# Performance work log

Measured on AMD Instinct MI355X. Metric: run time of the kernel, lower is better.

Reference implementation:

```python
import jax, jax.numpy as jnp
import numpy as np

B, N, C = 8, 1024, 10
RADIUS = 0.04
CONSUME_RADIUS = 0.04
ACCEL_SCALE = 0.02
MAX_VEL = 0.02
MAX_POS = 1.0
EDGES_TO_STAY_ALIVE = 3
CONSUME_EDGES_REQ = 1
EPS = 1e-9


def setup_inputs() -> dict:
    key = jax.random.key(0)
    ks = jax.random.split(key, 6)
    pos = jax.random.uniform(ks[0], (B, N, 2), dtype=jnp.float32) * 2.0 - 1.0  # in [-1, 1]
    vel = jax.random.normal(ks[1], (B, N, 2), dtype=jnp.float32) * 0.01
    # channel 4: node type, 1 = living cell, 0 = food (as in graph.x[:,4]==0 for food)
    cell = (jax.random.uniform(ks[2], (B, N, 1)) < 0.8).astype(jnp.float32)
    rest = jax.random.normal(ks[3], (B, N, C - 5), dtype=jnp.float32) * 0.1
    x = jnp.concatenate([pos, vel, cell, rest], axis=-1)  # [B,N,10]
    W1 = jax.random.normal(ks[4], (14, 16), dtype=jnp.float32) * 0.3
    W2 = jax.random.normal(ks[5], (16, 7), dtype=jnp.float32) * 0.3
    b1 = jnp.zeros((16,), jnp.float32)
    b2 = jnp.zeros((7,), jnp.float32)
    return {"x": x, "W1": W1, "b1": b1, "W2": W2, "b2": b2}


def reference(x, W1, b1, W2, b2):
    pos = x[..., :2]          # [B,N,2]
    vel = x[..., 2:4]         # [B,N,2]
    is_cell = x[..., 4] > 0.5  # [B,N] bool; food nodes have type 0
    cf = is_cell.astype(x.dtype)[..., None]  # [B,N,1]

    # ---- add_edges: dynamic radius graph (dense per-graph form) ----
    rel = pos[:, None, :, :] - pos[:, :, None, :]   # rel[b,i,j] = pos_j - pos_i, [B,N,N,2]
    dist = jnp.sqrt(jnp.sum(rel * rel, axis=-1) + EPS)  # [B,N,N]
    adj = (dist < RADIUS) & (dist > 1e-6)           # no self-edges
    adjf = adj.astype(x.dtype)

    # edge_attr = [dist, dx, dy, type_of_target]  (edge_attr[:,3]==0 -> food edge)
    tgt_type = jnp.broadcast_to(x[:, None, :, 4], dist.shape)
    e = jnp.stack([dist, rel[..., 0], rel[..., 1], tgt_type], axis=-1)  # [B,N,N,4]

    # ---- message_pass: MLP(concat(edge_attr, x_j)) -> hidden -> 7, sum-aggregate ----
    W1e, W1x = W1[:4], W1[4:]  # split so x_j term is computed once per node
    h = jax.nn.relu(
        jnp.einsum('bije,eh->bijh', e, W1e)
        + jnp.einsum('bjc,ch->bjh', x, W1x)[:, None, :, :]
        + b1
    )  # [B,N,N,16]
    agg_h = jnp.einsum('bij,bijh->bih', adjf, h)  # masked aggregation [B,N,16]
    deg = adjf.sum(-1)                            # [B,N]
    out = jnp.einsum('bih,ho->bio', agg_h, W2) + deg[..., None] * b2  # [B,N,7]

    # ---- update_graph: masked velocity / position scatter update ----
    out = out * cf  # h = message_pass(graph) * c_mask
    acc = out[..., :2] * ACCEL_SCALE
    new_vel = jnp.clip(vel + acc, -MAX_VEL, MAX_VEL)
    new_vel = jnp.where(is_cell[..., None], new_vel, vel)
    new_pos = jnp.clip(pos + new_vel * cf, -MAX_POS, MAX_POS)
    new_pos = jnp.where(is_cell[..., None], new_pos, pos)

    # ---- remove_nodes: island cells + consumed food -> keep mask (fixed shape) ----
    dead = is_cell & (deg < EDGES_TO_STAY_ALIVE)
    near = ((dist < CONSUME_RADIUS) & (dist > 1e-6)).astype(x.dtype)
    cell_neighbors = jnp.einsum('bij,bj->bi', near, cf[..., 0])  # cells near each node
    consumed = (~is_cell) & (cell_neighbors >= CONSUME_EDGES_REQ)
    keep = ~(dead | consumed)

    new_x = jnp.concatenate([new_pos, new_vel, x[..., 4:]], axis=-1)
    new_x = new_x * keep.astype(x.dtype)[..., None]  # prune by zeroing (fixed shape)
    return new_x
```

## Files before the change

### kernel.cpp

```cpp
#include <hip/hip_runtime.h>
#include <math.h>

namespace {

constexpr int BB = 8;
constexpr int NN = 1024;
constexpr int CC = 10;
constexpr float RADIUS = 0.04f;
constexpr float ACCEL_SCALE = 0.02f;
constexpr float MAX_VEL = 0.02f;
constexpr float MAX_POS = 1.0f;
constexpr float EPS = 1e-9f;
constexpr float D2_PREFILTER = 0.0017f;

__global__ __launch_bounds__(512) void gnca_one(
    const float* __restrict__ x,
    const float* __restrict__ W1,
    const float* __restrict__ b1,
    const float* __restrict__ W2,
    const float* __restrict__ b2,
    float* __restrict__ out)
{
    __shared__ alignas(16) float2 raw2[NN * 5];
    __shared__ alignas(16) float2 pos2[NN];

    const int tid = threadIdx.x;
    const int blk = blockIdx.x;
    const int b = blk >> 5;
    const int row0 = (blk & 31) * 32;
    const int w   = tid >> 6;
    const int sub = tid & 63;
    const int hh  = sub & 15;

    const float b1h = b1[hh];
    const float w1d = W1[hh];
    const float w1x = W1[16 + hh];
    const float w1y = W1[32 + hh];
    const float w1t = W1[48 + hh];
    float w1c[CC];
#pragma unroll
    for (int c = 0; c < CC; ++c) w1c[c] = W1[(4 + c) * 16 + hh];
    const float w20 = W2[hh * 7 + 0];
    const float w21 = W2[hh * 7 + 1];

    const float* __restrict__ xb = x + (size_t)b * NN * CC;

    {
        const float4* __restrict__ src = (const float4*)xb;
        float4* __restrict__ dst = (float4*)raw2;
#pragma unroll
        for (int k = 0; k < 5; ++k) dst[k * 512 + tid] = src[k * 512 + tid];
    }
    __syncthreads();

    {
        const float4* __restrict__ r4 = (const float4*)raw2;
        const float4 r0 = r4[tid * 5 + 0];
        const float4 r2 = r4[tid * 5 + 2];
        ((float4*)pos2)[tid] = make_float4(r0.x, r0.y, r2.z, r2.w);
    }
    __syncthreads();

    const int ibase = row0 + w * 4;
    float2 pi[4];
#pragma unroll
    for (int r = 0; r < 4; ++r) pi[r] = pos2[ibase + r];

    float o0p[4] = {0.f, 0.f, 0.f, 0.f};
    float o1p[4] = {0.f, 0.f, 0.f, 0.f};
    float dgp[4] = {0.f, 0.f, 0.f, 0.f};
    float cnp[4] = {0.f, 0.f, 0.f, 0.f};

    for (int jj = 0; jj < 16; ++jj) {
        const float2 pj = pos2[(jj << 6) + sub];

#pragma unroll
        for (int r = 0; r < 4; ++r) {
            const float dx = pj.x - pi[r].x;
            const float dy = pj.y - pi[r].y;
            unsigned long long m = __ballot(dx * dx + dy * dy < D2_PREFILTER);

            while (m) {
                const int src = __builtin_ctzll(m);
                m &= (m - 1);
                const int bj = (jj << 6) + src;
                const float2 q0 = raw2[bj * 5 + 0];
                const float2 q1 = raw2[bj * 5 + 1];
                const float2 q2 = raw2[bj * 5 + 2];
                const float2 q3 = raw2[bj * 5 + 3];
                const float2 q4 = raw2[bj * 5 + 4];
                const float bx = q0.x - pi[r].x;
                const float by = q0.y - pi[r].y;
                const float d2 =
                    __fadd_rn(__fadd_rn(__fmul_rn(bx, bx), __fmul_rn(by, by)), EPS);
                const float dist = __fsqrt_rn(d2);
                if (dist < RADIUS) {
                    const float tgt = q2.x;
                    float v = b1h;
                    v = fmaf(q0.x, w1c[0], v);  v = fmaf(q0.y, w1c[1], v);
                    v = fmaf(q1.x, w1c[2], v);  v = fmaf(q1.y, w1c[3], v);
                    v = fmaf(q2.x, w1c[4], v);  v = fmaf(q2.y, w1c[5], v);
                    v = fmaf(q3.x, w1c[6], v);  v = fmaf(q3.y, w1c[7], v);
                    v = fmaf(q4.x, w1c[8], v);  v = fmaf(q4.y, w1c[9], v);
                    v = fmaf(tgt,  w1t, v);
                    v = fmaf(by,   w1y, v);
                    v = fmaf(bx,   w1x, v);
                    v = fmaf(dist, w1d, v);
                    v = fmaxf(v, 0.0f);
                    o0p[r] = fmaf(v, w20, o0p[r]);
                    o1p[r] = fmaf(v, w21, o1p[r]);
                    dgp[r] += 1.0f;
                    cnp[r] += (tgt > 0.5f) ? 1.0f : 0.0f;
                }
            }
        }
    }

#pragma unroll
    for (int mm = 1; mm < 16; mm <<= 1) {
#pragma unroll
        for (int r = 0; r < 4; ++r) {
            o0p[r] += __shfl_xor(o0p[r], mm, 64);
            o1p[r] += __shfl_xor(o1p[r], mm, 64);
        }
    }

    if (sub < 4) {
        float o0s = o0p[0], o1s = o1p[0], degs = dgp[0], cns = cnp[0];
        float2 pis = pi[0];
#pragma unroll
        for (int r = 1; r < 4; ++r) {
            if (sub == r) {
                o0s = o0p[r]; o1s = o1p[r]; degs = dgp[r]; cns = cnp[r];
                pis = pi[r];
            }
        }
        const int iu = ibase + sub;

        const float2 q1 = raw2[iu * 5 + 1];
        const float2 q2 = raw2[iu * 5 + 2];
        const float2 q3 = raw2[iu * 5 + 3];
        const float2 q4 = raw2[iu * 5 + 4];

        const float typ_i = q2.x;
        const bool is_cell = typ_i > 0.5f;

        float o0 = degs * b2[0] + o0s;
        float o1 = degs * b2[1] + o1s;
        if (!is_cell) { o0 = 0.0f; o1 = 0.0f; }

        float nvx = q1.x, nvy = q1.y;
        float npx = pis.x, npy = pis.y;
        if (is_cell) {
            nvx = fminf(fmaxf(q1.x + o0 * ACCEL_SCALE, -MAX_VEL), MAX_VEL);
            nvy = fminf(fmaxf(q1.y + o1 * ACCEL_SCALE, -MAX_VEL), MAX_VEL);
            npx = fminf(fmaxf(pis.x + nvx, -MAX_POS), MAX_POS);
            npy = fminf(fmaxf(pis.y + nvy, -MAX_POS), MAX_POS);
        }

        const bool dead     = is_cell && (degs < 3.0f);
        const bool consumed = (!is_cell) && (cns >= 1.0f);
        const float keep = (dead || consumed) ? 0.0f : 1.0f;

        float2* __restrict__ op2 = (float2*)(out + ((size_t)b * NN + iu) * CC);
        op2[0] = make_float2(npx * keep, npy * keep);
        op2[1] = make_float2(nvx * keep, nvy * keep);
        op2[2] = make_float2(typ_i * keep, q2.y * keep);
        op2[3] = make_float2(q3.x * keep, q3.y * keep);
        op2[4] = make_float2(q4.x * keep, q4.y * keep);
    }
}

}

extern "C" void kernel_launch(void* const* d_in, const int* in_sizes, int n_in,
                              void* d_out, int out_size, void* d_ws, size_t ws_size,
                              hipStream_t stream) {
    const float* x  = (const float*)d_in[0];
    const float* W1 = (const float*)d_in[1];
    const float* b1 = (const float*)d_in[2];
    const float* W2 = (const float*)d_in[3];
    const float* b2 = (const float*)d_in[4];
    float* out = (float*)d_out;

    gnca_one<<<dim3(256), dim3(512), 0, stream>>>(x, W1, b1, W2, b2, out);
}
```

Baseline: 13.39 us.

## Assign one row per wavefront and launch four times more blocks

Each wavefront now handles a single target row instead of four, and the grid grows from 256 to 1024 blocks, each covering 8 rows. Position loads for the column sweep are batched eight at a time so their latency overlaps the ballot work. This spreads the work over more of the GPU's compute units and shortens the serial per-wave loop. The cost is that each block still stages the whole 40KB graph into shared memory, so global-to-LDS traffic is four times higher, and the larger LDS footprint per row may limit occupancy.

```diff
diff --git a/kernel.cpp b/kernel.cpp
--- a/kernel.cpp
+++ b/kernel.cpp
@@ -26,8 +26,8 @@
 
     const int tid = threadIdx.x;
     const int blk = blockIdx.x;
-    const int b = blk >> 5;
-    const int row0 = (blk & 31) * 32;
+    const int b = blk >> 7;
+    const int row0 = (blk & 127) * 8;
     const int w   = tid >> 6;
     const int sub = tid & 63;
     const int hh  = sub & 15;
@@ -61,23 +61,24 @@
     }
     __syncthreads();
 
-    const int ibase = row0 + w * 4;
-    float2 pi[4];
-#pragma unroll
-    for (int r = 0; r < 4; ++r) pi[r] = pos2[ibase + r];
+    const int iu = row0 + w;
+    const float2 pi = pos2[iu];
 
-    float o0p[4] = {0.f, 0.f, 0.f, 0.f};
-    float o1p[4] = {0.f, 0.f, 0.f, 0.f};
-    float dgp[4] = {0.f, 0.f, 0.f, 0.f};
-    float cnp[4] = {0.f, 0.f, 0.f, 0.f};
-
-    for (int jj = 0; jj < 16; ++jj) {
-        const float2 pj = pos2[(jj << 6) + sub];
+    float o0p = 0.0f, o1p = 0.0f, dg = 0.0f, cn = 0.0f;
 
 #pragma unroll
-        for (int r = 0; r < 4; ++r) {
-            const float dx = pj.x - pi[r].x;
-            const float dy = pj.y - pi[r].y;
+    for (int g = 0; g < 2; ++g) {
+        float2 pjv[8];
+#pragma unroll
+        for (int q = 0; q < 8; ++q)
+            pjv[q] = pos2[(((g << 3) + q) << 6) + sub];
+
+#pragma unroll
+        for (int q = 0; q < 8; ++q) {
+            const int jj = (g << 3) + q;
+            const float2 pj = pjv[q];
+            const float dx = pj.x - pi.x;
+            const float dy = pj.y - pi.y;
             unsigned long long m = __ballot(dx * dx + dy * dy < D2_PREFILTER);
 
             while (m) {
@@ -89,8 +90,8 @@
                 const float2 q2 = raw2[bj * 5 + 2];
                 const float2 q3 = raw2[bj * 5 + 3];
                 const float2 q4 = raw2[bj * 5 + 4];
-                const float bx = q0.x - pi[r].x;
-                const float by = q0.y - pi[r].y;
+                const float bx = q0.x - pi.x;
+                const float by = q0.y - pi.y;
                 const float d2 =
                     __fadd_rn(__fadd_rn(__fmul_rn(bx, bx), __fmul_rn(by, by)), EPS);
                 const float dist = __fsqrt_rn(d2);
@@ -107,10 +108,10 @@
                     v = fmaf(bx,   w1x, v);
                     v = fmaf(dist, w1d, v);
                     v = fmaxf(v, 0.0f);
-                    o0p[r] = fmaf(v, w20, o0p[r]);
-                    o1p[r] = fmaf(v, w21, o1p[r]);
-                    dgp[r] += 1.0f;
-                    cnp[r] += (tgt > 0.5f) ? 1.0f : 0.0f;
+                    o0p = fmaf(v, w20, o0p);
+                    o1p = fmaf(v, w21, o1p);
+                    dg += 1.0f;
+                    cn += (tgt > 0.5f) ? 1.0f : 0.0f;
                 }
             }
         }
@@ -118,25 +119,11 @@
 
 #pragma unroll
     for (int mm = 1; mm < 16; mm <<= 1) {
-#pragma unroll
-        for (int r = 0; r < 4; ++r) {
-            o0p[r] += __shfl_xor(o0p[r], mm, 64);
-            o1p[r] += __shfl_xor(o1p[r], mm, 64);
-        }
+        o0p += __shfl_xor(o0p, mm, 64);
+        o1p += __shfl_xor(o1p, mm, 64);
     }
 
-    if (sub < 4) {
-        float o0s = o0p[0], o1s = o1p[0], degs = dgp[0], cns = cnp[0];
-        float2 pis = pi[0];
-#pragma unroll
-        for (int r = 1; r < 4; ++r) {
-            if (sub == r) {
-                o0s = o0p[r]; o1s = o1p[r]; degs = dgp[r]; cns = cnp[r];
-                pis = pi[r];
-            }
-        }
-        const int iu = ibase + sub;
-
+    if (sub == 0) {
         const float2 q1 = raw2[iu * 5 + 1];
         const float2 q2 = raw2[iu * 5 + 2];
         const float2 q3 = raw2[iu * 5 + 3];
@@ -145,21 +132,21 @@
         const float typ_i = q2.x;
         const bool is_cell = typ_i > 0.5f;
 
-        float o0 = degs * b2[0] + o0s;
-        float o1 = degs * b2[1] + o1s;
+        float o0 = dg * b2[0] + o0p;
+        float o1 = dg * b2[1] + o1p;
         if (!is_cell) { o0 = 0.0f; o1 = 0.0f; }
 
         float nvx = q1.x, nvy = q1.y;
-        float npx = pis.x, npy = pis.y;
+        float npx = pi.x, npy = pi.y;
         if (is_cell) {
             nvx = fminf(fmaxf(q1.x + o0 * ACCEL_SCALE, -MAX_VEL), MAX_VEL);
             nvy = fminf(fmaxf(q1.y + o1 * ACCEL_SCALE, -MAX_VEL), MAX_VEL);
-            npx = fminf(fmaxf(pis.x + nvx, -MAX_POS), MAX_POS);
-            npy = fminf(fmaxf(pis.y + nvy, -MAX_POS), MAX_POS);
+            npx = fminf(fmaxf(pi.x + nvx, -MAX_POS), MAX_POS);
+            npy = fminf(fmaxf(pi.y + nvy, -MAX_POS), MAX_POS);
         }
 
-        const bool dead     = is_cell && (degs < 3.0f);
-        const bool consumed = (!is_cell) && (cns >= 1.0f);
+        const bool dead     = is_cell && (dg < 3.0f);
+        const bool consumed = (!is_cell) && (cn >= 1.0f);
         const float keep = (dead || consumed) ? 0.0f : 1.0f;
 
         float2* __restrict__ op2 = (float2*)(out + ((size_t)b * NN + iu) * CC);
@@ -183,5 +170,5 @@
     const float* b2 = (const float*)d_in[4];
     float* out = (float*)d_out;
 
-    gnca_one<<<dim3(256), dim3(512), 0, stream>>>(x, W1, b1, W2, b2, out);
+    gnca_one<<<dim3(BB * 128), dim3(512), 0, stream>>>(x, W1, b1, W2, b2, out);
 }
```

Result: no change. 13.20 us (-1.4%).
